# Optimization experiments

Hardware: AMD Instinct MI355X
Metric: run time of the kernel (lower is better)

The kernel has to match this reference:

```python
import jax, jax.numpy as jnp
import numpy as np

N_NODES = 100000
N_EDGES = 1600000
D_FEAT = 128
N_CLASS = 40
K_HOPS = 2  # nlayers


def setup_inputs() -> dict:
    key = jax.random.key(0)
    k1, k2, k3, k4, k5 = jax.random.split(key, 5)
    src = jax.random.randint(k1, (N_EDGES,), 0, N_NODES)
    dst = jax.random.randint(k2, (N_EDGES,), 0, N_NODES)
    features = jax.random.normal(k3, (N_NODES, D_FEAT), dtype=jnp.float32)
    # positive edge weights (EdgeWeightNorm requires nonnegative)
    edge_weight = jax.random.uniform(k4, (N_EDGES,), dtype=jnp.float32, minval=0.1, maxval=1.0)
    W = jax.random.normal(k5, (D_FEAT, N_CLASS), dtype=jnp.float32) / np.float32(np.sqrt(D_FEAT))
    b = jnp.zeros((N_CLASS,), dtype=jnp.float32)
    return {"features": features, "src": src, "dst": dst,
            "edge_weight": edge_weight, "W": W, "b": b}


def reference(features, src, dst, edge_weight, W, b):
    """SGConv (DGL) with edge_weight: EdgeWeightNorm('both') then k SpMM hops, then fc."""
    n = features.shape[0]
    # EdgeWeightNorm('both'): w_ij / sqrt(out_deg_w(src_i) * in_deg_w(dst_j))
    out_deg = jax.ops.segment_sum(edge_weight, src, num_segments=n)  # weighted out-degree
    in_deg = jax.ops.segment_sum(edge_weight, dst, num_segments=n)   # weighted in-degree
    w = edge_weight * jax.lax.rsqrt(out_deg[src]) * jax.lax.rsqrt(in_deg[dst])  # [E]
    h = features
    for _ in range(K_HOPS):
        # message = h[src] * w ; aggregate = scatter-sum over dst
        h = jax.ops.segment_sum(h[src] * w[:, None], dst, num_segments=n)  # [N, D]
    return h @ W + b  # fc projection [N, C]
```

## Files before the change

### kernel.cpp

```cpp
#include <hip/hip_runtime.h>

#define N_NODES 100000
#define N_EDGES 1600000
#define D_FEAT  128
#define N_CLASS 40
#define ELL_CAP 48

#define QS  10239.6875f
#define DQ  9.765923e-5f
#define FSC  2048.0f
#define FINV (1.0f/2048.0f)
#define CNT_SHIFT 20
#define W_MASK ((1u << CNT_SHIFT) - 1u)

#define RSZ 20000
#define NR 5
#define SLICES 32
#define EPS (N_EDGES/SLICES)
#define HB (NR*SLICES)

#define GEMM4_T ((N_NODES/4)*(N_CLASS/4))
#define GEMM4_B ((GEMM4_T + 1023)/1024)

#define NCH 5

__device__ __forceinline__ float bf_lo(unsigned int u) { return __uint_as_float(u << 16); }
__device__ __forceinline__ float bf_hi(unsigned int u) { return __uint_as_float(u & 0xFFFF0000u); }
__device__ __forceinline__ unsigned int bf_pack2(float a, float b) {
    unsigned int ua = __float_as_uint(a), ub = __float_as_uint(b);
    ua = (ua + 0x7FFFu + ((ua >> 16) & 1u)) >> 16;
    ub = (ub + 0x7FFFu + ((ub >> 16) & 1u)) & 0xFFFF0000u;
    return ua | ub;
}

__global__ __launch_bounds__(1024, 8) void mega1_kernel(
    const int* __restrict__ src, const int* __restrict__ dst, const float* __restrict__ ew,
    const float* __restrict__ f, const float* __restrict__ W,
    unsigned int* __restrict__ dhist, unsigned int* __restrict__ shist,
    unsigned int* __restrict__ g0)
{
    __shared__ unsigned int smem[RSZ];
    const int b = blockIdx.x;
    const int tid = threadIdx.x;

    if (b < 2 * HB) {
        const bool isDst = (b < HB);
        const int b2 = isDst ? b : b - HB;
        const int* idxarr = isDst ? dst : src;
        unsigned int* outh = isDst ? dhist : shist;
        int r = b2 / SLICES, s = b2 - r * SLICES;
        int nb = r * RSZ;
        for (int i = tid; i < RSZ; i += 1024) smem[i] = 0u;
        __syncthreads();
        int e0 = s * EPS;
        const int4*   idx4 = (const int4*)(idxarr + e0);
        const float4* ew4  = (const float4*)(ew + e0);
        const unsigned int cbit = isDst ? (1u << CNT_SHIFT) : 0u;
        for (int i = tid; i < EPS / 8; i += 1024) {
            int4   ia = idx4[2 * i],     ib = idx4[2 * i + 1];
            float4 wa = ew4[2 * i],      wb = ew4[2 * i + 1];
            unsigned int r0 = (unsigned int)(ia.x - nb);
            unsigned int r1 = (unsigned int)(ia.y - nb);
            unsigned int r2 = (unsigned int)(ia.z - nb);
            unsigned int r3 = (unsigned int)(ia.w - nb);
            unsigned int r4 = (unsigned int)(ib.x - nb);
            unsigned int r5 = (unsigned int)(ib.y - nb);
            unsigned int r6 = (unsigned int)(ib.z - nb);
            unsigned int r7 = (unsigned int)(ib.w - nb);
            if (r0 < RSZ) atomicAdd(&smem[r0], cbit | (unsigned int)(wa.x * FSC + 0.5f));
            if (r1 < RSZ) atomicAdd(&smem[r1], cbit | (unsigned int)(wa.y * FSC + 0.5f));
            if (r2 < RSZ) atomicAdd(&smem[r2], cbit | (unsigned int)(wa.z * FSC + 0.5f));
            if (r3 < RSZ) atomicAdd(&smem[r3], cbit | (unsigned int)(wa.w * FSC + 0.5f));
            if (r4 < RSZ) atomicAdd(&smem[r4], cbit | (unsigned int)(wb.x * FSC + 0.5f));
            if (r5 < RSZ) atomicAdd(&smem[r5], cbit | (unsigned int)(wb.y * FSC + 0.5f));
            if (r6 < RSZ) atomicAdd(&smem[r6], cbit | (unsigned int)(wb.z * FSC + 0.5f));
            if (r7 < RSZ) atomicAdd(&smem[r7], cbit | (unsigned int)(wb.w * FSC + 0.5f));
        }
        __syncthreads();
        unsigned int* o = outh + (size_t)b2 * RSZ;
        for (int i = tid; i < RSZ; i += 1024) o[i] = smem[i];
    } else {
        float* Ws = (float*)smem;
        for (int i = tid; i < D_FEAT * N_CLASS; i += 1024) Ws[i] = W[i];
        __syncthreads();
        int idx = (b - 2 * HB) * 1024 + tid;
        if (idx >= GEMM4_T) return;
        int n4 = idx / (N_CLASS / 4);
        int c4i = idx - n4 * (N_CLASS / 4);
        int c4 = c4i * 4;
        int n0 = n4 * 4;
        const float* fr0 = f + (size_t)n0 * D_FEAT;
        float4 acc0 = {0.f, 0.f, 0.f, 0.f};
        float4 acc1 = {0.f, 0.f, 0.f, 0.f};
        float4 acc2 = {0.f, 0.f, 0.f, 0.f};
        float4 acc3 = {0.f, 0.f, 0.f, 0.f};
#pragma unroll 1
        for (int kq = 0; kq < D_FEAT; kq += 4) {
            float4 fv0 = *(const float4*)(fr0 + kq);
            float4 fv1 = *(const float4*)(fr0 + D_FEAT + kq);
            float4 fv2 = *(const float4*)(fr0 + 2 * D_FEAT + kq);
            float4 fv3 = *(const float4*)(fr0 + 3 * D_FEAT + kq);
#pragma unroll
            for (int j = 0; j < 4; ++j) {
                float fa = (j == 0) ? fv0.x : (j == 1) ? fv0.y : (j == 2) ? fv0.z : fv0.w;
                float fb = (j == 0) ? fv1.x : (j == 1) ? fv1.y : (j == 2) ? fv1.z : fv1.w;
                float fc = (j == 0) ? fv2.x : (j == 1) ? fv2.y : (j == 2) ? fv2.z : fv2.w;
                float fd = (j == 0) ? fv3.x : (j == 1) ? fv3.y : (j == 2) ? fv3.z : fv3.w;
                const float4 wv = *(const float4*)&Ws[(kq + j) * N_CLASS + c4];
                acc0.x = fmaf(fa, wv.x, acc0.x); acc0.y = fmaf(fa, wv.y, acc0.y);
                acc0.z = fmaf(fa, wv.z, acc0.z); acc0.w = fmaf(fa, wv.w, acc0.w);
                acc1.x = fmaf(fb, wv.x, acc1.x); acc1.y = fmaf(fb, wv.y, acc1.y);
                acc1.z = fmaf(fb, wv.z, acc1.z); acc1.w = fmaf(fb, wv.w, acc1.w);
                acc2.x = fmaf(fc, wv.x, acc2.x); acc2.y = fmaf(fc, wv.y, acc2.y);
                acc2.z = fmaf(fc, wv.z, acc2.z); acc2.w = fmaf(fc, wv.w, acc2.w);
                acc3.x = fmaf(fd, wv.x, acc3.x); acc3.y = fmaf(fd, wv.y, acc3.y);
                acc3.z = fmaf(fd, wv.z, acc3.z); acc3.w = fmaf(fd, wv.w, acc3.w);
            }
        }
        uint2 p0, p1, p2, p3;
        p0.x = bf_pack2(acc0.x, acc0.y); p0.y = bf_pack2(acc0.z, acc0.w);
        p1.x = bf_pack2(acc1.x, acc1.y); p1.y = bf_pack2(acc1.z, acc1.w);
        p2.x = bf_pack2(acc2.x, acc2.y); p2.y = bf_pack2(acc2.z, acc2.w);
        p3.x = bf_pack2(acc3.x, acc3.y); p3.y = bf_pack2(acc3.z, acc3.w);
        *(uint2*)&g0[(size_t)n0 * (N_CLASS / 2) + c4i * 2] = p0;
        *(uint2*)&g0[(size_t)(n0 + 1) * (N_CLASS / 2) + c4i * 2] = p1;
        *(uint2*)&g0[(size_t)(n0 + 2) * (N_CLASS / 2) + c4i * 2] = p2;
        *(uint2*)&g0[(size_t)(n0 + 3) * (N_CLASS / 2) + c4i * 2] = p3;
    }
}

__global__ __launch_bounds__(256) void scan_kernel(
    const unsigned int* __restrict__ dhist, const unsigned int* __restrict__ shist,
    unsigned char* __restrict__ base8, int* __restrict__ cnt,
    float* __restrict__ rs_out, float* __restrict__ rs_in,
    unsigned int* __restrict__ ell)
{
    __shared__ unsigned int owp[256], iwp[256], cntp[256];
    int t = blockIdx.x * 256 + threadIdx.x;
    int n = t >> 2, q = t & 3;
    bool valid = n < N_NODES;
    unsigned int ow = 0, iw = 0, tot = 0;
    unsigned int c0=0,c1=0,c2=0,c3=0,c4=0,c5=0,c6=0,c7=0;
    const unsigned int* dp = nullptr;
    unsigned char* b8 = nullptr;
    if (valid) {
        int r = n / RSZ, off = n - r * RSZ;
        dp = dhist + (size_t)r * SLICES * RSZ + off + (size_t)(q * 8) * RSZ;
        const unsigned int* sp = shist + (size_t)r * SLICES * RSZ + off + (size_t)(q * 8) * RSZ;
        b8 = base8 + (size_t)r * SLICES * RSZ + off + (size_t)(q * 8) * RSZ;
        unsigned int d0 = dp[0],        d1 = dp[(size_t)RSZ],     d2 = dp[(size_t)2*RSZ], d3 = dp[(size_t)3*RSZ];
        unsigned int d4 = dp[(size_t)4*RSZ], d5 = dp[(size_t)5*RSZ], d6 = dp[(size_t)6*RSZ], d7 = dp[(size_t)7*RSZ];
        unsigned int s0 = sp[0],        s1 = sp[(size_t)RSZ],     s2 = sp[(size_t)2*RSZ], s3 = sp[(size_t)3*RSZ];
        unsigned int s4 = sp[(size_t)4*RSZ], s5 = sp[(size_t)5*RSZ], s6 = sp[(size_t)6*RSZ], s7 = sp[(size_t)7*RSZ];
        ow = s0+s1+s2+s3+s4+s5+s6+s7;
        iw = (d0&W_MASK)+(d1&W_MASK)+(d2&W_MASK)+(d3&W_MASK)
           + (d4&W_MASK)+(d5&W_MASK)+(d6&W_MASK)+(d7&W_MASK);
        c0 = d0>>CNT_SHIFT; c1 = d1>>CNT_SHIFT; c2 = d2>>CNT_SHIFT; c3 = d3>>CNT_SHIFT;
        c4 = d4>>CNT_SHIFT; c5 = d5>>CNT_SHIFT; c6 = d6>>CNT_SHIFT; c7 = d7>>CNT_SHIFT;
        tot = c0+c1+c2+c3+c4+c5+c6+c7;
    }
    owp[threadIdx.x] = ow; iwp[threadIdx.x] = iw; cntp[threadIdx.x] = tot;
    __syncthreads();
    if (!valid) return;
    int b0 = threadIdx.x & ~3;
    unsigned int base = 0;
    if (q > 0) base += cntp[b0];
    if (q > 1) base += cntp[b0 + 1];
    if (q > 2) base += cntp[b0 + 2];
    unsigned int p = base;
    b8[0] = (unsigned char)p; p += c0;
    b8[(size_t)RSZ]   = (unsigned char)p; p += c1;
    b8[(size_t)2*RSZ] = (unsigned char)p; p += c2;
    b8[(size_t)3*RSZ] = (unsigned char)p; p += c3;
    b8[(size_t)4*RSZ] = (unsigned char)p; p += c4;
    b8[(size_t)5*RSZ] = (unsigned char)p; p += c5;
    b8[(size_t)6*RSZ] = (unsigned char)p; p += c6;
    b8[(size_t)7*RSZ] = (unsigned char)p;
    if (q == 0) {
        unsigned int owt = owp[b0] + owp[b0+1] + owp[b0+2] + owp[b0+3];
        unsigned int iwt = iwp[b0] + iwp[b0+1] + iwp[b0+2] + iwp[b0+3];
        unsigned int run = cntp[b0] + cntp[b0+1] + cntp[b0+2] + cntp[b0+3];
        rs_out[n] = owt ? rsqrtf((float)owt * FINV) : 0.f;
        rs_in[n]  = iwt ? rsqrtf((float)iwt * FINV) : 0.f;
        cnt[n] = (int)run;
        int k  = min((int)run, ELL_CAP);
        int k8 = min((k + 7) & ~7, ELL_CAP);
        unsigned int* row = ell + (size_t)n * ELL_CAP;
        for (int i = k; i < k8; ++i) row[i] = 0u;
    }
}

__global__ __launch_bounds__(1024) void fill_kernel(
    const int* __restrict__ src, const int* __restrict__ dst, const float* __restrict__ ew,
    const unsigned char* __restrict__ base8, const float* __restrict__ rs_out,
    unsigned int* __restrict__ ell)
{
    __shared__ unsigned int lds[RSZ];
    const int r = blockIdx.x & 7;
    const int s = blockIdx.x >> 3;
    if (r >= NR) return;
    const int tid = threadIdx.x;
    const int b2 = r * SLICES + s;
    int nb = r * RSZ;
    const unsigned int* bp = (const unsigned int*)(base8 + (size_t)b2 * RSZ);
    for (int i = tid; i < RSZ / 4; i += 1024) {
        unsigned int v = bp[i];
        lds[4 * i]     = v & 255u;
        lds[4 * i + 1] = (v >> 8) & 255u;
        lds[4 * i + 2] = (v >> 16) & 255u;
        lds[4 * i + 3] = v >> 24;
    }
    __syncthreads();
    int e0 = s * EPS;
    const int4*   d4 = (const int4*)(dst + e0);
    const int4*   s4 = (const int4*)(src + e0);
    const float4* w4 = (const float4*)(ew + e0);
    for (int i = tid; i < EPS / 8; i += 1024) {
        int4   da = d4[2 * i], db = d4[2 * i + 1];
        int4   sa = s4[2 * i], sb = s4[2 * i + 1];
        float4 wa = w4[2 * i], wb = w4[2 * i + 1];
#pragma unroll
        for (int j = 0; j < 8; ++j) {
            int d, sn; float w;
            switch (j) {
                case 0: d = da.x; sn = sa.x; w = wa.x; break;
                case 1: d = da.y; sn = sa.y; w = wa.y; break;
                case 2: d = da.z; sn = sa.z; w = wa.z; break;
                case 3: d = da.w; sn = sa.w; w = wa.w; break;
                case 4: d = db.x; sn = sb.x; w = wb.x; break;
                case 5: d = db.y; sn = sb.y; w = wb.y; break;
                case 6: d = db.z; sn = sb.z; w = wb.z; break;
                default: d = db.w; sn = sb.w; w = wb.w; break;
            }
            unsigned int rr = (unsigned int)(d - nb);
            if (rr < RSZ) {
                unsigned int slot = atomicAdd(&lds[rr], 1u);
                if (slot < ELL_CAP) {
                    int q = (int)(w * rs_out[sn] * QS + 0.5f);
                    q = q > 32767 ? 32767 : q;
                    ell[(size_t)d * ELL_CAP + slot] = ((unsigned int)sn << 15) | (unsigned int)q;
                }
            }
        }
    }
}

__global__ void hop_kernel(const unsigned int* __restrict__ ell, const int* __restrict__ cnt,
                           const float* __restrict__ rs_in, const unsigned int* __restrict__ gin,
                           void* __restrict__ gout, const float* __restrict__ bias)
{
    int t = blockIdx.x * 256 + threadIdx.x;
    if (t >= N_NODES * NCH) return;
    int n = t / NCH;
    int c8 = t - n * NCH;
    int k = min(cnt[n], ELL_CAP);
    k = (k + 7) & ~7;
    const uint4* row4 = (const uint4*)(ell + (size_t)n * ELL_CAP);
    const uint4* gin4 = (const uint4*)gin;
    float a0 = 0.f, a1 = 0.f, a2 = 0.f, a3 = 0.f, a4 = 0.f, a5 = 0.f, a6 = 0.f, a7 = 0.f;
    for (int i = 0; i < k; i += 8) {
        uint4 v0 = row4[i >> 2];
        uint4 v1 = row4[(i >> 2) + 1];
        unsigned int e0 = v0.x, e1 = v0.y, e2 = v0.z, e3 = v0.w;
        unsigned int e4 = v1.x, e5 = v1.y, e6 = v1.z, e7 = v1.w;
        uint4 g0v = gin4[(size_t)(e0 >> 15) * NCH + c8];
        uint4 g1v = gin4[(size_t)(e1 >> 15) * NCH + c8];
        uint4 g2v = gin4[(size_t)(e2 >> 15) * NCH + c8];
        uint4 g3v = gin4[(size_t)(e3 >> 15) * NCH + c8];
        uint4 g4v = gin4[(size_t)(e4 >> 15) * NCH + c8];
        uint4 g5v = gin4[(size_t)(e5 >> 15) * NCH + c8];
        uint4 g6v = gin4[(size_t)(e6 >> 15) * NCH + c8];
        uint4 g7v = gin4[(size_t)(e7 >> 15) * NCH + c8];
        float w0 = (float)(e0 & 32767u) * DQ;
        float w1 = (float)(e1 & 32767u) * DQ;
        float w2 = (float)(e2 & 32767u) * DQ;
        float w3 = (float)(e3 & 32767u) * DQ;
        float w4 = (float)(e4 & 32767u) * DQ;
        float w5 = (float)(e5 & 32767u) * DQ;
        float w6 = (float)(e6 & 32767u) * DQ;
        float w7 = (float)(e7 & 32767u) * DQ;
        a0 = fmaf(w0, bf_lo(g0v.x), a0); a1 = fmaf(w0, bf_hi(g0v.x), a1);
        a2 = fmaf(w0, bf_lo(g0v.y), a2); a3 = fmaf(w0, bf_hi(g0v.y), a3);
        a4 = fmaf(w0, bf_lo(g0v.z), a4); a5 = fmaf(w0, bf_hi(g0v.z), a5);
        a6 = fmaf(w0, bf_lo(g0v.w), a6); a7 = fmaf(w0, bf_hi(g0v.w), a7);
        a0 = fmaf(w1, bf_lo(g1v.x), a0); a1 = fmaf(w1, bf_hi(g1v.x), a1);
        a2 = fmaf(w1, bf_lo(g1v.y), a2); a3 = fmaf(w1, bf_hi(g1v.y), a3);
        a4 = fmaf(w1, bf_lo(g1v.z), a4); a5 = fmaf(w1, bf_hi(g1v.z), a5);
        a6 = fmaf(w1, bf_lo(g1v.w), a6); a7 = fmaf(w1, bf_hi(g1v.w), a7);
        a0 = fmaf(w2, bf_lo(g2v.x), a0); a1 = fmaf(w2, bf_hi(g2v.x), a1);
        a2 = fmaf(w2, bf_lo(g2v.y), a2); a3 = fmaf(w2, bf_hi(g2v.y), a3);
        a4 = fmaf(w2, bf_lo(g2v.z), a4); a5 = fmaf(w2, bf_hi(g2v.z), a5);
        a6 = fmaf(w2, bf_lo(g2v.w), a6); a7 = fmaf(w2, bf_hi(g2v.w), a7);
        a0 = fmaf(w3, bf_lo(g3v.x), a0); a1 = fmaf(w3, bf_hi(g3v.x), a1);
        a2 = fmaf(w3, bf_lo(g3v.y), a2); a3 = fmaf(w3, bf_hi(g3v.y), a3);
        a4 = fmaf(w3, bf_lo(g3v.z), a4); a5 = fmaf(w3, bf_hi(g3v.z), a5);
        a6 = fmaf(w3, bf_lo(g3v.w), a6); a7 = fmaf(w3, bf_hi(g3v.w), a7);
        a0 = fmaf(w4, bf_lo(g4v.x), a0); a1 = fmaf(w4, bf_hi(g4v.x), a1);
        a2 = fmaf(w4, bf_lo(g4v.y), a2); a3 = fmaf(w4, bf_hi(g4v.y), a3);
        a4 = fmaf(w4, bf_lo(g4v.z), a4); a5 = fmaf(w4, bf_hi(g4v.z), a5);
        a6 = fmaf(w4, bf_lo(g4v.w), a6); a7 = fmaf(w4, bf_hi(g4v.w), a7);
        a0 = fmaf(w5, bf_lo(g5v.x), a0); a1 = fmaf(w5, bf_hi(g5v.x), a1);
        a2 = fmaf(w5, bf_lo(g5v.y), a2); a3 = fmaf(w5, bf_hi(g5v.y), a3);
        a4 = fmaf(w5, bf_lo(g5v.z), a4); a5 = fmaf(w5, bf_hi(g5v.z), a5);
        a6 = fmaf(w5, bf_lo(g5v.w), a6); a7 = fmaf(w5, bf_hi(g5v.w), a7);
        a0 = fmaf(w6, bf_lo(g6v.x), a0); a1 = fmaf(w6, bf_hi(g6v.x), a1);
        a2 = fmaf(w6, bf_lo(g6v.y), a2); a3 = fmaf(w6, bf_hi(g6v.y), a3);
        a4 = fmaf(w6, bf_lo(g6v.z), a4); a5 = fmaf(w6, bf_hi(g6v.z), a5);
        a6 = fmaf(w6, bf_lo(g6v.w), a6); a7 = fmaf(w6, bf_hi(g6v.w), a7);
        a0 = fmaf(w7, bf_lo(g7v.x), a0); a1 = fmaf(w7, bf_hi(g7v.x), a1);
        a2 = fmaf(w7, bf_lo(g7v.y), a2); a3 = fmaf(w7, bf_hi(g7v.y), a3);
        a4 = fmaf(w7, bf_lo(g7v.z), a4); a5 = fmaf(w7, bf_hi(g7v.z), a5);
        a6 = fmaf(w7, bf_lo(g7v.w), a6); a7 = fmaf(w7, bf_hi(g7v.w), a7);
    }
    float sc = rs_in[n];
    a0 *= sc; a1 *= sc; a2 *= sc; a3 *= sc; a4 *= sc; a5 *= sc; a6 *= sc; a7 *= sc;
    if (bias) {
        const float4 b0 = *(const float4*)&bias[c8 * 8];
        const float4 b1 = *(const float4*)&bias[c8 * 8 + 4];
        float4 o0 = {a0 + b0.x, a1 + b0.y, a2 + b0.z, a3 + b0.w};
        float4 o1 = {a4 + b1.x, a5 + b1.y, a6 + b1.z, a7 + b1.w};
        float* op = (float*)gout + (size_t)n * N_CLASS + c8 * 8;
        *(float4*)op = o0;
        *(float4*)(op + 4) = o1;
    } else {
        uint4 p;
        p.x = bf_pack2(a0, a1);
        p.y = bf_pack2(a2, a3);
        p.z = bf_pack2(a4, a5);
        p.w = bf_pack2(a6, a7);
        ((uint4*)gout)[(size_t)n * NCH + c8] = p;
    }
}

extern "C" void kernel_launch(void* const* d_in, const int* in_sizes, int n_in,
                              void* d_out, int out_size, void* d_ws, size_t ws_size,
                              hipStream_t stream) {
    const float* features = (const float*)d_in[0];
    const int*   src      = (const int*)d_in[1];
    const int*   dst      = (const int*)d_in[2];
    const float* ew       = (const float*)d_in[3];
    const float* W        = (const float*)d_in[4];
    const float* b        = (const float*)d_in[5];
    float*       out      = (float*)d_out;

    char* ws = (char*)d_ws;
    unsigned int* dhist = (unsigned int*)ws;  ws += (size_t)HB * RSZ * 4;
    unsigned int* shist = (unsigned int*)ws;  ws += (size_t)HB * RSZ * 4;
    unsigned char* base8 = (unsigned char*)ws; ws += (size_t)HB * RSZ;
    int*   cnt    = (int*)ws;    ws += (size_t)N_NODES * 4;
    float* rs_out = (float*)ws;  ws += (size_t)N_NODES * 4;
    float* rs_in  = (float*)ws;  ws += (size_t)N_NODES * 4;
    unsigned int* ell = (unsigned int*)ws; ws += (size_t)N_NODES * ELL_CAP * 4;
    unsigned int* g0  = (unsigned int*)ws;
    unsigned int* g1  = dhist;

    const int B = 256;

    mega1_kernel<<<2 * HB + GEMM4_B, 1024, 0, stream>>>(
        src, dst, ew, features, W, dhist, shist, g0);
    scan_kernel<<<(N_NODES * 4 + B - 1) / B, B, 0, stream>>>(
        dhist, shist, base8, cnt, rs_out, rs_in, ell);
    fill_kernel<<<8 * SLICES, 1024, 0, stream>>>(src, dst, ew, base8, rs_out, ell);

    const int HOP_BLOCKS = (N_NODES * NCH + B - 1) / B;
    hop_kernel<<<HOP_BLOCKS, B, 0, stream>>>(ell, cnt, rs_in, g0, (void*)g1, nullptr);
    hop_kernel<<<HOP_BLOCKS, B, 0, stream>>>(ell, cnt, rs_in, g1, (void*)out, b);
}
```

Baseline: 271.9 us.

## Move feature GEMM from histogram kernel into ELL fill kernel

The dense features×W projection is moved out of the histogram kernel and co-scheduled with the ELL fill kernel as extra blocks, so its work overlaps the atomic-heavy fill instead of the histogram pass. Each GEMM thread now computes 2 node rows instead of 4, doubling the GEMM block count for more parallelism. The histogram kernel also drops its occupancy hint in launch_bounds. The trade-off is that the fill kernel carries extra LDS and register pressure from the GEMM branch.

```diff
diff --git a/kernel.cpp b/kernel.cpp
--- a/kernel.cpp
+++ b/kernel.cpp
@@ -19,8 +19,10 @@
 #define EPS (N_EDGES/SLICES)
 #define HB (NR*SLICES)
 
-#define GEMM4_T ((N_NODES/4)*(N_CLASS/4))
-#define GEMM4_B ((GEMM4_T + 1023)/1024)
+#define GEMM2_T ((N_NODES/2)*(N_CLASS/4))
+#define GEMM2_B ((GEMM2_T + 1023)/1024)
+
+#define FILLB 256
 
 #define NCH 5
 
@@ -33,100 +35,48 @@
     return ua | ub;
 }
 
-__global__ __launch_bounds__(1024, 8) void mega1_kernel(
+__global__ __launch_bounds__(1024) void mega1_kernel(
     const int* __restrict__ src, const int* __restrict__ dst, const float* __restrict__ ew,
-    const float* __restrict__ f, const float* __restrict__ W,
-    unsigned int* __restrict__ dhist, unsigned int* __restrict__ shist,
-    unsigned int* __restrict__ g0)
+    unsigned int* __restrict__ dhist, unsigned int* __restrict__ shist)
 {
     __shared__ unsigned int smem[RSZ];
     const int b = blockIdx.x;
     const int tid = threadIdx.x;
-
-    if (b < 2 * HB) {
-        const bool isDst = (b < HB);
-        const int b2 = isDst ? b : b - HB;
-        const int* idxarr = isDst ? dst : src;
-        unsigned int* outh = isDst ? dhist : shist;
-        int r = b2 / SLICES, s = b2 - r * SLICES;
-        int nb = r * RSZ;
-        for (int i = tid; i < RSZ; i += 1024) smem[i] = 0u;
-        __syncthreads();
-        int e0 = s * EPS;
-        const int4*   idx4 = (const int4*)(idxarr + e0);
-        const float4* ew4  = (const float4*)(ew + e0);
-        const unsigned int cbit = isDst ? (1u << CNT_SHIFT) : 0u;
-        for (int i = tid; i < EPS / 8; i += 1024) {
-            int4   ia = idx4[2 * i],     ib = idx4[2 * i + 1];
-            float4 wa = ew4[2 * i],      wb = ew4[2 * i + 1];
-            unsigned int r0 = (unsigned int)(ia.x - nb);
-            unsigned int r1 = (unsigned int)(ia.y - nb);
-            unsigned int r2 = (unsigned int)(ia.z - nb);
-            unsigned int r3 = (unsigned int)(ia.w - nb);
-            unsigned int r4 = (unsigned int)(ib.x - nb);
-            unsigned int r5 = (unsigned int)(ib.y - nb);
-            unsigned int r6 = (unsigned int)(ib.z - nb);
-            unsigned int r7 = (unsigned int)(ib.w - nb);
-            if (r0 < RSZ) atomicAdd(&smem[r0], cbit | (unsigned int)(wa.x * FSC + 0.5f));
-            if (r1 < RSZ) atomicAdd(&smem[r1], cbit | (unsigned int)(wa.y * FSC + 0.5f));
-            if (r2 < RSZ) atomicAdd(&smem[r2], cbit | (unsigned int)(wa.z * FSC + 0.5f));
-            if (r3 < RSZ) atomicAdd(&smem[r3], cbit | (unsigned int)(wa.w * FSC + 0.5f));
-            if (r4 < RSZ) atomicAdd(&smem[r4], cbit | (unsigned int)(wb.x * FSC + 0.5f));
-            if (r5 < RSZ) atomicAdd(&smem[r5], cbit | (unsigned int)(wb.y * FSC + 0.5f));
-            if (r6 < RSZ) atomicAdd(&smem[r6], cbit | (unsigned int)(wb.z * FSC + 0.5f));
-            if (r7 < RSZ) atomicAdd(&smem[r7], cbit | (unsigned int)(wb.w * FSC + 0.5f));
-        }
-        __syncthreads();
-        unsigned int* o = outh + (size_t)b2 * RSZ;
-        for (int i = tid; i < RSZ; i += 1024) o[i] = smem[i];
-    } else {
-        float* Ws = (float*)smem;
-        for (int i = tid; i < D_FEAT * N_CLASS; i += 1024) Ws[i] = W[i];
-        __syncthreads();
-        int idx = (b - 2 * HB) * 1024 + tid;
-        if (idx >= GEMM4_T) return;
-        int n4 = idx / (N_CLASS / 4);
-        int c4i = idx - n4 * (N_CLASS / 4);
-        int c4 = c4i * 4;
-        int n0 = n4 * 4;
-        const float* fr0 = f + (size_t)n0 * D_FEAT;
-        float4 acc0 = {0.f, 0.f, 0.f, 0.f};
-        float4 acc1 = {0.f, 0.f, 0.f, 0.f};
-        float4 acc2 = {0.f, 0.f, 0.f, 0.f};
-        float4 acc3 = {0.f, 0.f, 0.f, 0.f};
-#pragma unroll 1
-        for (int kq = 0; kq < D_FEAT; kq += 4) {
-            float4 fv0 = *(const float4*)(fr0 + kq);
-            float4 fv1 = *(const float4*)(fr0 + D_FEAT + kq);
-            float4 fv2 = *(const float4*)(fr0 + 2 * D_FEAT + kq);
-            float4 fv3 = *(const float4*)(fr0 + 3 * D_FEAT + kq);
-#pragma unroll
-            for (int j = 0; j < 4; ++j) {
-                float fa = (j == 0) ? fv0.x : (j == 1) ? fv0.y : (j == 2) ? fv0.z : fv0.w;
-                float fb = (j == 0) ? fv1.x : (j == 1) ? fv1.y : (j == 2) ? fv1.z : fv1.w;
-                float fc = (j == 0) ? fv2.x : (j == 1) ? fv2.y : (j == 2) ? fv2.z : fv2.w;
-                float fd = (j == 0) ? fv3.x : (j == 1) ? fv3.y : (j == 2) ? fv3.z : fv3.w;
-                const float4 wv = *(const float4*)&Ws[(kq + j) * N_CLASS + c4];
-                acc0.x = fmaf(fa, wv.x, acc0.x); acc0.y = fmaf(fa, wv.y, acc0.y);
-                acc0.z = fmaf(fa, wv.z, acc0.z); acc0.w = fmaf(fa, wv.w, acc0.w);
-                acc1.x = fmaf(fb, wv.x, acc1.x); acc1.y = fmaf(fb, wv.y, acc1.y);
-                acc1.z = fmaf(fb, wv.z, acc1.z); acc1.w = fmaf(fb, wv.w, acc1.w);
-                acc2.x = fmaf(fc, wv.x, acc2.x); acc2.y = fmaf(fc, wv.y, acc2.y);
-                acc2.z = fmaf(fc, wv.z, acc2.z); acc2.w = fmaf(fc, wv.w, acc2.w);
-                acc3.x = fmaf(fd, wv.x, acc3.x); acc3.y = fmaf(fd, wv.y, acc3.y);
-                acc3.z = fmaf(fd, wv.z, acc3.z); acc3.w = fmaf(fd, wv.w, acc3.w);
-            }
-        }
-        uint2 p0, p1, p2, p3;
-        p0.x = bf_pack2(acc0.x, acc0.y); p0.y = bf_pack2(acc0.z, acc0.w);
-        p1.x = bf_pack2(acc1.x, acc1.y); p1.y = bf_pack2(acc1.z, acc1.w);
-        p2.x = bf_pack2(acc2.x, acc2.y); p2.y = bf_pack2(acc2.z, acc2.w);
-        p3.x = bf_pack2(acc3.x, acc3.y); p3.y = bf_pack2(acc3.z, acc3.w);
-        *(uint2*)&g0[(size_t)n0 * (N_CLASS / 2) + c4i * 2] = p0;
-        *(uint2*)&g0[(size_t)(n0 + 1) * (N_CLASS / 2) + c4i * 2] = p1;
-        *(uint2*)&g0[(size_t)(n0 + 2) * (N_CLASS / 2) + c4i * 2] = p2;
-        *(uint2*)&g0[(size_t)(n0 + 3) * (N_CLASS / 2) + c4i * 2] = p3;
-    }
+    const bool isDst = (b < HB);
+    const int b2 = isDst ? b : b - HB;
+    const int* idxarr = isDst ? dst : src;
+    unsigned int* outh = isDst ? dhist : shist;
+    int r = b2 / SLICES, s = b2 - r * SLICES;
+    int nb = r * RSZ;
+    for (int i = tid; i < RSZ; i += 1024) smem[i] = 0u;
+    __syncthreads();
+    int e0 = s * EPS;
+    const int4*   idx4 = (const int4*)(idxarr + e0);
+    const float4* ew4  = (const float4*)(ew + e0);
+    const unsigned int cbit = isDst ? (1u << CNT_SHIFT) : 0u;
+    for (int i = tid; i < EPS / 8; i += 1024) {
+        int4   ia = idx4[2 * i],     ib = idx4[2 * i + 1];
+        float4 wa = ew4[2 * i],      wb = ew4[2 * i + 1];
+        unsigned int r0 = (unsigned int)(ia.x - nb);
+        unsigned int r1 = (unsigned int)(ia.y - nb);
+        unsigned int r2 = (unsigned int)(ia.z - nb);
+        unsigned int r3 = (unsigned int)(ia.w - nb);
+        unsigned int r4 = (unsigned int)(ib.x - nb);
+        unsigned int r5 = (unsigned int)(ib.y - nb);
+        unsigned int r6 = (unsigned int)(ib.z - nb);
+        unsigned int r7 = (unsigned int)(ib.w - nb);
+        if (r0 < RSZ) atomicAdd(&smem[r0], cbit | (unsigned int)(wa.x * FSC + 0.5f));
+        if (r1 < RSZ) atomicAdd(&smem[r1], cbit | (unsigned int)(wa.y * FSC + 0.5f));
+        if (r2 < RSZ) atomicAdd(&smem[r2], cbit | (unsigned int)(wa.z * FSC + 0.5f));
+        if (r3 < RSZ) atomicAdd(&smem[r3], cbit | (unsigned int)(wa.w * FSC + 0.5f));
+        if (r4 < RSZ) atomicAdd(&smem[r4], cbit | (unsigned int)(wb.x * FSC + 0.5f));
+        if (r5 < RSZ) atomicAdd(&smem[r5], cbit | (unsigned int)(wb.y * FSC + 0.5f));
+        if (r6 < RSZ) atomicAdd(&smem[r6], cbit | (unsigned int)(wb.z * FSC + 0.5f));
+        if (r7 < RSZ) atomicAdd(&smem[r7], cbit | (unsigned int)(wb.w * FSC + 0.5f));
+    }
+    __syncthreads();
+    unsigned int* o = outh + (size_t)b2 * RSZ;
+    for (int i = tid; i < RSZ; i += 1024) o[i] = smem[i];
 }
 
 __global__ __launch_bounds__(256) void scan_kernel(
@@ -141,11 +91,10 @@
     bool valid = n < N_NODES;
     unsigned int ow = 0, iw = 0, tot = 0;
     unsigned int c0=0,c1=0,c2=0,c3=0,c4=0,c5=0,c6=0,c7=0;
-    const unsigned int* dp = nullptr;
     unsigned char* b8 = nullptr;
     if (valid) {
         int r = n / RSZ, off = n - r * RSZ;
-        dp = dhist + (size_t)r * SLICES * RSZ + off + (size_t)(q * 8) * RSZ;
+        const unsigned int* dp = dhist + (size_t)r * SLICES * RSZ + off + (size_t)(q * 8) * RSZ;
         const unsigned int* sp = shist + (size_t)r * SLICES * RSZ + off + (size_t)(q * 8) * RSZ;
         b8 = base8 + (size_t)r * SLICES * RSZ + off + (size_t)(q * 8) * RSZ;
         unsigned int d0 = dp[0],        d1 = dp[(size_t)RSZ],     d2 = dp[(size_t)2*RSZ], d3 = dp[(size_t)3*RSZ];
@@ -190,58 +139,98 @@
     }
 }
 
-__global__ __launch_bounds__(1024) void fill_kernel(
+__global__ __launch_bounds__(1024) void fill_gemm_kernel(
     const int* __restrict__ src, const int* __restrict__ dst, const float* __restrict__ ew,
     const unsigned char* __restrict__ base8, const float* __restrict__ rs_out,
-    unsigned int* __restrict__ ell)
+    unsigned int* __restrict__ ell,
+    const float* __restrict__ f, const float* __restrict__ W,
+    unsigned int* __restrict__ g0)
 {
     __shared__ unsigned int lds[RSZ];
-    const int r = blockIdx.x & 7;
-    const int s = blockIdx.x >> 3;
-    if (r >= NR) return;
+    const int b = blockIdx.x;
     const int tid = threadIdx.x;
-    const int b2 = r * SLICES + s;
-    int nb = r * RSZ;
-    const unsigned int* bp = (const unsigned int*)(base8 + (size_t)b2 * RSZ);
-    for (int i = tid; i < RSZ / 4; i += 1024) {
-        unsigned int v = bp[i];
-        lds[4 * i]     = v & 255u;
-        lds[4 * i + 1] = (v >> 8) & 255u;
-        lds[4 * i + 2] = (v >> 16) & 255u;
-        lds[4 * i + 3] = v >> 24;
-    }
-    __syncthreads();
-    int e0 = s * EPS;
-    const int4*   d4 = (const int4*)(dst + e0);
-    const int4*   s4 = (const int4*)(src + e0);
-    const float4* w4 = (const float4*)(ew + e0);
-    for (int i = tid; i < EPS / 8; i += 1024) {
-        int4   da = d4[2 * i], db = d4[2 * i + 1];
-        int4   sa = s4[2 * i], sb = s4[2 * i + 1];
-        float4 wa = w4[2 * i], wb = w4[2 * i + 1];
+
+    if (b < FILLB) {
+        const int r = b & 7;
+        const int s = b >> 3;
+        if (r >= NR) return;
+        const int b2 = r * SLICES + s;
+        int nb = r * RSZ;
+        const unsigned int* bp = (const unsigned int*)(base8 + (size_t)b2 * RSZ);
+        for (int i = tid; i < RSZ / 4; i += 1024) {
+            unsigned int v = bp[i];
+            lds[4 * i]     = v & 255u;
+            lds[4 * i + 1] = (v >> 8) & 255u;
+            lds[4 * i + 2] = (v >> 16) & 255u;
+            lds[4 * i + 3] = v >> 24;
+        }
+        __syncthreads();
+        int e0 = s * EPS;
+        const int4*   d4 = (const int4*)(dst + e0);
+        const int4*   s4 = (const int4*)(src + e0);
+        const float4* w4 = (const float4*)(ew + e0);
+        for (int i = tid; i < EPS / 8; i += 1024) {
+            int4   da = d4[2 * i], db = d4[2 * i + 1];
+            int4   sa = s4[2 * i], sb = s4[2 * i + 1];
+            float4 wa = w4[2 * i], wb = w4[2 * i + 1];
 #pragma unroll
-        for (int j = 0; j < 8; ++j) {
-            int d, sn; float w;
-            switch (j) {
-                case 0: d = da.x; sn = sa.x; w = wa.x; break;
-                case 1: d = da.y; sn = sa.y; w = wa.y; break;
-                case 2: d = da.z; sn = sa.z; w = wa.z; break;
-                case 3: d = da.w; sn = sa.w; w = wa.w; break;
-                case 4: d = db.x; sn = sb.x; w = wb.x; break;
-                case 5: d = db.y; sn = sb.y; w = wb.y; break;
-                case 6: d = db.z; sn = sb.z; w = wb.z; break;
-                default: d = db.w; sn = sb.w; w = wb.w; break;
-            }
-            unsigned int rr = (unsigned int)(d - nb);
-            if (rr < RSZ) {
-                unsigned int slot = atomicAdd(&lds[rr], 1u);
-                if (slot < ELL_CAP) {
-                    int q = (int)(w * rs_out[sn] * QS + 0.5f);
-                    q = q > 32767 ? 32767 : q;
-                    ell[(size_t)d * ELL_CAP + slot] = ((unsigned int)sn << 15) | (unsigned int)q;
+            for (int j = 0; j < 8; ++j) {
+                int d, sn; float w;
+                switch (j) {
+                    case 0: d = da.x; sn = sa.x; w = wa.x; break;
+                    case 1: d = da.y; sn = sa.y; w = wa.y; break;
+                    case 2: d = da.z; sn = sa.z; w = wa.z; break;
+                    case 3: d = da.w; sn = sa.w; w = wa.w; break;
+                    case 4: d = db.x; sn = sb.x; w = wb.x; break;
+                    case 5: d = db.y; sn = sb.y; w = wb.y; break;
+                    case 6: d = db.z; sn = sb.z; w = wb.z; break;
+                    default: d = db.w; sn = sb.w; w = wb.w; break;
+                }
+                unsigned int rr = (unsigned int)(d - nb);
+                if (rr < RSZ) {
+                    unsigned int slot = atomicAdd(&lds[rr], 1u);
+                    if (slot < ELL_CAP) {
+                        int q = (int)(w * rs_out[sn] * QS + 0.5f);
+                        q = q > 32767 ? 32767 : q;
+                        ell[(size_t)d * ELL_CAP + slot] = ((unsigned int)sn << 15) | (unsigned int)q;
+                    }
                 }
             }
         }
+    } else {
+        float* Ws = (float*)lds;
+        for (int i = tid; i < D_FEAT * N_CLASS; i += 1024) Ws[i] = W[i];
+        __syncthreads();
+        int idx = (b - FILLB) * 1024 + tid;
+        if (idx >= GEMM2_T) return;
+        int n2 = idx / (N_CLASS / 4);
+        int c4i = idx - n2 * (N_CLASS / 4);
+        int c4 = c4i * 4;
+        int n0 = n2 * 2;
+        const float* fr0 = f + (size_t)n0 * D_FEAT;
+        const float* fr1 = fr0 + D_FEAT;
+        float4 acc0 = {0.f, 0.f, 0.f, 0.f};
+        float4 acc1 = {0.f, 0.f, 0.f, 0.f};
+#pragma unroll 1
+        for (int kq = 0; kq < D_FEAT; kq += 4) {
+            float4 fv0 = *(const float4*)(fr0 + kq);
+            float4 fv1 = *(const float4*)(fr1 + kq);
+#pragma unroll
+            for (int j = 0; j < 4; ++j) {
+                float fa = (j == 0) ? fv0.x : (j == 1) ? fv0.y : (j == 2) ? fv0.z : fv0.w;
+                float fb = (j == 0) ? fv1.x : (j == 1) ? fv1.y : (j == 2) ? fv1.z : fv1.w;
+                const float4 wv = *(const float4*)&Ws[(kq + j) * N_CLASS + c4];
+                acc0.x = fmaf(fa, wv.x, acc0.x); acc0.y = fmaf(fa, wv.y, acc0.y);
+                acc0.z = fmaf(fa, wv.z, acc0.z); acc0.w = fmaf(fa, wv.w, acc0.w);
+                acc1.x = fmaf(fb, wv.x, acc1.x); acc1.y = fmaf(fb, wv.y, acc1.y);
+                acc1.z = fmaf(fb, wv.z, acc1.z); acc1.w = fmaf(fb, wv.w, acc1.w);
+            }
+        }
+        uint2 p0, p1;
+        p0.x = bf_pack2(acc0.x, acc0.y); p0.y = bf_pack2(acc0.z, acc0.w);
+        p1.x = bf_pack2(acc1.x, acc1.y); p1.y = bf_pack2(acc1.z, acc1.w);
+        *(uint2*)&g0[(size_t)n0 * (N_CLASS / 2) + c4i * 2] = p0;
+        *(uint2*)&g0[(size_t)(n0 + 1) * (N_CLASS / 2) + c4i * 2] = p1;
     }
 }
 
@@ -356,11 +345,11 @@
 
     const int B = 256;
 
-    mega1_kernel<<<2 * HB + GEMM4_B, 1024, 0, stream>>>(
-        src, dst, ew, features, W, dhist, shist, g0);
+    mega1_kernel<<<2 * HB, 1024, 0, stream>>>(src, dst, ew, dhist, shist);
     scan_kernel<<<(N_NODES * 4 + B - 1) / B, B, 0, stream>>>(
         dhist, shist, base8, cnt, rs_out, rs_in, ell);
-    fill_kernel<<<8 * SLICES, 1024, 0, stream>>>(src, dst, ew, base8, rs_out, ell);
+    fill_gemm_kernel<<<FILLB + GEMM2_B, 1024, 0, stream>>>(
+        src, dst, ew, base8, rs_out, ell, features, W, g0);
 
     const int HOP_BLOCKS = (N_NODES * NCH + B - 1) / B;
     hop_kernel<<<HOP_BLOCKS, B, 0, stream>>>(ell, cnt, rs_in, g0, (void*)g1, nullptr);
```

New measurement: 275.0 us. About the same (+1.1%).

## Split GEMM out of histogram megakernel and shrink histogram range size

Applied to the files above, without the earlier changes.

Moves the feature-times-W projection out of the fused histogram kernel into its own 256-thread kernel launched after the fill pass. The histogram range size drops from 20000 to 12500 nodes over 8 ranges, so the LDS footprint per block shrinks and the fill kernel's 8-range grid is now fully used. The goal is higher occupancy and lighter LDS pressure for the histogram blocks, at the cost of an extra launch, more histogram blocks that each rescan their edge slice, and the loss of overlap between the GEMM and the histogram work.

```diff
diff --git a/kernel.cpp b/kernel.cpp
--- a/kernel.cpp
+++ b/kernel.cpp
@@ -13,14 +13,14 @@
 #define CNT_SHIFT 20
 #define W_MASK ((1u << CNT_SHIFT) - 1u)
 
-#define RSZ 20000
-#define NR 5
+#define RSZ 12500
+#define NR 8
 #define SLICES 32
 #define EPS (N_EDGES/SLICES)
 #define HB (NR*SLICES)
 
 #define GEMM4_T ((N_NODES/4)*(N_CLASS/4))
-#define GEMM4_B ((GEMM4_T + 1023)/1024)
+#define GEMM4_B ((GEMM4_T + 255)/256)
 
 #define NCH 5
 
@@ -33,100 +33,48 @@
     return ua | ub;
 }
 
-__global__ __launch_bounds__(1024, 8) void mega1_kernel(
+__global__ __launch_bounds__(1024) void mega1_kernel(
     const int* __restrict__ src, const int* __restrict__ dst, const float* __restrict__ ew,
-    const float* __restrict__ f, const float* __restrict__ W,
-    unsigned int* __restrict__ dhist, unsigned int* __restrict__ shist,
-    unsigned int* __restrict__ g0)
+    unsigned int* __restrict__ dhist, unsigned int* __restrict__ shist)
 {
     __shared__ unsigned int smem[RSZ];
     const int b = blockIdx.x;
     const int tid = threadIdx.x;
-
-    if (b < 2 * HB) {
-        const bool isDst = (b < HB);
-        const int b2 = isDst ? b : b - HB;
-        const int* idxarr = isDst ? dst : src;
-        unsigned int* outh = isDst ? dhist : shist;
-        int r = b2 / SLICES, s = b2 - r * SLICES;
-        int nb = r * RSZ;
-        for (int i = tid; i < RSZ; i += 1024) smem[i] = 0u;
-        __syncthreads();
-        int e0 = s * EPS;
-        const int4*   idx4 = (const int4*)(idxarr + e0);
-        const float4* ew4  = (const float4*)(ew + e0);
-        const unsigned int cbit = isDst ? (1u << CNT_SHIFT) : 0u;
-        for (int i = tid; i < EPS / 8; i += 1024) {
-            int4   ia = idx4[2 * i],     ib = idx4[2 * i + 1];
-            float4 wa = ew4[2 * i],      wb = ew4[2 * i + 1];
-            unsigned int r0 = (unsigned int)(ia.x - nb);
-            unsigned int r1 = (unsigned int)(ia.y - nb);
-            unsigned int r2 = (unsigned int)(ia.z - nb);
-            unsigned int r3 = (unsigned int)(ia.w - nb);
-            unsigned int r4 = (unsigned int)(ib.x - nb);
-            unsigned int r5 = (unsigned int)(ib.y - nb);
-            unsigned int r6 = (unsigned int)(ib.z - nb);
-            unsigned int r7 = (unsigned int)(ib.w - nb);
-            if (r0 < RSZ) atomicAdd(&smem[r0], cbit | (unsigned int)(wa.x * FSC + 0.5f));
-            if (r1 < RSZ) atomicAdd(&smem[r1], cbit | (unsigned int)(wa.y * FSC + 0.5f));
-            if (r2 < RSZ) atomicAdd(&smem[r2], cbit | (unsigned int)(wa.z * FSC + 0.5f));
-            if (r3 < RSZ) atomicAdd(&smem[r3], cbit | (unsigned int)(wa.w * FSC + 0.5f));
-            if (r4 < RSZ) atomicAdd(&smem[r4], cbit | (unsigned int)(wb.x * FSC + 0.5f));
-            if (r5 < RSZ) atomicAdd(&smem[r5], cbit | (unsigned int)(wb.y * FSC + 0.5f));
-            if (r6 < RSZ) atomicAdd(&smem[r6], cbit | (unsigned int)(wb.z * FSC + 0.5f));
-            if (r7 < RSZ) atomicAdd(&smem[r7], cbit | (unsigned int)(wb.w * FSC + 0.5f));
-        }
-        __syncthreads();
-        unsigned int* o = outh + (size_t)b2 * RSZ;
-        for (int i = tid; i < RSZ; i += 1024) o[i] = smem[i];
-    } else {
-        float* Ws = (float*)smem;
-        for (int i = tid; i < D_FEAT * N_CLASS; i += 1024) Ws[i] = W[i];
-        __syncthreads();
-        int idx = (b - 2 * HB) * 1024 + tid;
-        if (idx >= GEMM4_T) return;
-        int n4 = idx / (N_CLASS / 4);
-        int c4i = idx - n4 * (N_CLASS / 4);
-        int c4 = c4i * 4;
-        int n0 = n4 * 4;
-        const float* fr0 = f + (size_t)n0 * D_FEAT;
-        float4 acc0 = {0.f, 0.f, 0.f, 0.f};
-        float4 acc1 = {0.f, 0.f, 0.f, 0.f};
-        float4 acc2 = {0.f, 0.f, 0.f, 0.f};
-        float4 acc3 = {0.f, 0.f, 0.f, 0.f};
-#pragma unroll 1
-        for (int kq = 0; kq < D_FEAT; kq += 4) {
-            float4 fv0 = *(const float4*)(fr0 + kq);
-            float4 fv1 = *(const float4*)(fr0 + D_FEAT + kq);
-            float4 fv2 = *(const float4*)(fr0 + 2 * D_FEAT + kq);
-            float4 fv3 = *(const float4*)(fr0 + 3 * D_FEAT + kq);
-#pragma unroll
-            for (int j = 0; j < 4; ++j) {
-                float fa = (j == 0) ? fv0.x : (j == 1) ? fv0.y : (j == 2) ? fv0.z : fv0.w;
-                float fb = (j == 0) ? fv1.x : (j == 1) ? fv1.y : (j == 2) ? fv1.z : fv1.w;
-                float fc = (j == 0) ? fv2.x : (j == 1) ? fv2.y : (j == 2) ? fv2.z : fv2.w;
-                float fd = (j == 0) ? fv3.x : (j == 1) ? fv3.y : (j == 2) ? fv3.z : fv3.w;
-                const float4 wv = *(const float4*)&Ws[(kq + j) * N_CLASS + c4];
-                acc0.x = fmaf(fa, wv.x, acc0.x); acc0.y = fmaf(fa, wv.y, acc0.y);
-                acc0.z = fmaf(fa, wv.z, acc0.z); acc0.w = fmaf(fa, wv.w, acc0.w);
-                acc1.x = fmaf(fb, wv.x, acc1.x); acc1.y = fmaf(fb, wv.y, acc1.y);
-                acc1.z = fmaf(fb, wv.z, acc1.z); acc1.w = fmaf(fb, wv.w, acc1.w);
-                acc2.x = fmaf(fc, wv.x, acc2.x); acc2.y = fmaf(fc, wv.y, acc2.y);
-                acc2.z = fmaf(fc, wv.z, acc2.z); acc2.w = fmaf(fc, wv.w, acc2.w);
-                acc3.x = fmaf(fd, wv.x, acc3.x); acc3.y = fmaf(fd, wv.y, acc3.y);
-                acc3.z = fmaf(fd, wv.z, acc3.z); acc3.w = fmaf(fd, wv.w, acc3.w);
-            }
-        }
-        uint2 p0, p1, p2, p3;
-        p0.x = bf_pack2(acc0.x, acc0.y); p0.y = bf_pack2(acc0.z, acc0.w);
-        p1.x = bf_pack2(acc1.x, acc1.y); p1.y = bf_pack2(acc1.z, acc1.w);
-        p2.x = bf_pack2(acc2.x, acc2.y); p2.y = bf_pack2(acc2.z, acc2.w);
-        p3.x = bf_pack2(acc3.x, acc3.y); p3.y = bf_pack2(acc3.z, acc3.w);
-        *(uint2*)&g0[(size_t)n0 * (N_CLASS / 2) + c4i * 2] = p0;
-        *(uint2*)&g0[(size_t)(n0 + 1) * (N_CLASS / 2) + c4i * 2] = p1;
-        *(uint2*)&g0[(size_t)(n0 + 2) * (N_CLASS / 2) + c4i * 2] = p2;
-        *(uint2*)&g0[(size_t)(n0 + 3) * (N_CLASS / 2) + c4i * 2] = p3;
-    }
+    const bool isDst = (b < HB);
+    const int b2 = isDst ? b : b - HB;
+    const int* idxarr = isDst ? dst : src;
+    unsigned int* outh = isDst ? dhist : shist;
+    int r = b2 / SLICES, s = b2 - r * SLICES;
+    int nb = r * RSZ;
+    for (int i = tid; i < RSZ; i += 1024) smem[i] = 0u;
+    __syncthreads();
+    int e0 = s * EPS;
+    const int4*   idx4 = (const int4*)(idxarr + e0);
+    const float4* ew4  = (const float4*)(ew + e0);
+    const unsigned int cbit = isDst ? (1u << CNT_SHIFT) : 0u;
+    for (int i = tid; i < EPS / 8; i += 1024) {
+        int4   ia = idx4[2 * i],     ib = idx4[2 * i + 1];
+        float4 wa = ew4[2 * i],      wb = ew4[2 * i + 1];
+        unsigned int r0 = (unsigned int)(ia.x - nb);
+        unsigned int r1 = (unsigned int)(ia.y - nb);
+        unsigned int r2 = (unsigned int)(ia.z - nb);
+        unsigned int r3 = (unsigned int)(ia.w - nb);
+        unsigned int r4 = (unsigned int)(ib.x - nb);
+        unsigned int r5 = (unsigned int)(ib.y - nb);
+        unsigned int r6 = (unsigned int)(ib.z - nb);
+        unsigned int r7 = (unsigned int)(ib.w - nb);
+        if (r0 < RSZ) atomicAdd(&smem[r0], cbit | (unsigned int)(wa.x * FSC + 0.5f));
+        if (r1 < RSZ) atomicAdd(&smem[r1], cbit | (unsigned int)(wa.y * FSC + 0.5f));
+        if (r2 < RSZ) atomicAdd(&smem[r2], cbit | (unsigned int)(wa.z * FSC + 0.5f));
+        if (r3 < RSZ) atomicAdd(&smem[r3], cbit | (unsigned int)(wa.w * FSC + 0.5f));
+        if (r4 < RSZ) atomicAdd(&smem[r4], cbit | (unsigned int)(wb.x * FSC + 0.5f));
+        if (r5 < RSZ) atomicAdd(&smem[r5], cbit | (unsigned int)(wb.y * FSC + 0.5f));
+        if (r6 < RSZ) atomicAdd(&smem[r6], cbit | (unsigned int)(wb.z * FSC + 0.5f));
+        if (r7 < RSZ) atomicAdd(&smem[r7], cbit | (unsigned int)(wb.w * FSC + 0.5f));
+    }
+    __syncthreads();
+    unsigned int* o = outh + (size_t)b2 * RSZ;
+    for (int i = tid; i < RSZ; i += 1024) o[i] = smem[i];
 }
 
 __global__ __launch_bounds__(256) void scan_kernel(
@@ -140,24 +88,24 @@
     int n = t >> 2, q = t & 3;
     bool valid = n < N_NODES;
     unsigned int ow = 0, iw = 0, tot = 0;
-    unsigned int c0=0,c1=0,c2=0,c3=0,c4=0,c5=0,c6=0,c7=0;
-    const unsigned int* dp = nullptr;
+    unsigned int dv[8];
     unsigned char* b8 = nullptr;
+#pragma unroll
+    for (int j = 0; j < 8; ++j) dv[j] = 0u;
     if (valid) {
         int r = n / RSZ, off = n - r * RSZ;
-        dp = dhist + (size_t)r * SLICES * RSZ + off + (size_t)(q * 8) * RSZ;
+        const unsigned int* dp = dhist + (size_t)r * SLICES * RSZ + off + (size_t)(q * 8) * RSZ;
         const unsigned int* sp = shist + (size_t)r * SLICES * RSZ + off + (size_t)(q * 8) * RSZ;
         b8 = base8 + (size_t)r * SLICES * RSZ + off + (size_t)(q * 8) * RSZ;
-        unsigned int d0 = dp[0],        d1 = dp[(size_t)RSZ],     d2 = dp[(size_t)2*RSZ], d3 = dp[(size_t)3*RSZ];
-        unsigned int d4 = dp[(size_t)4*RSZ], d5 = dp[(size_t)5*RSZ], d6 = dp[(size_t)6*RSZ], d7 = dp[(size_t)7*RSZ];
-        unsigned int s0 = sp[0],        s1 = sp[(size_t)RSZ],     s2 = sp[(size_t)2*RSZ], s3 = sp[(size_t)3*RSZ];
-        unsigned int s4 = sp[(size_t)4*RSZ], s5 = sp[(size_t)5*RSZ], s6 = sp[(size_t)6*RSZ], s7 = sp[(size_t)7*RSZ];
-        ow = s0+s1+s2+s3+s4+s5+s6+s7;
-        iw = (d0&W_MASK)+(d1&W_MASK)+(d2&W_MASK)+(d3&W_MASK)
-           + (d4&W_MASK)+(d5&W_MASK)+(d6&W_MASK)+(d7&W_MASK);
-        c0 = d0>>CNT_SHIFT; c1 = d1>>CNT_SHIFT; c2 = d2>>CNT_SHIFT; c3 = d3>>CNT_SHIFT;
-        c4 = d4>>CNT_SHIFT; c5 = d5>>CNT_SHIFT; c6 = d6>>CNT_SHIFT; c7 = d7>>CNT_SHIFT;
-        tot = c0+c1+c2+c3+c4+c5+c6+c7;
+        unsigned int sv[8];
+#pragma unroll
+        for (int j = 0; j < 8; ++j) dv[j] = dp[(size_t)j * RSZ];
+#pragma unroll
+        for (int j = 0; j < 8; ++j) sv[j] = sp[(size_t)j * RSZ];
+#pragma unroll
+        for (int j = 0; j < 8; ++j) ow += sv[j];
+#pragma unroll
+        for (int j = 0; j < 8; ++j) { iw += dv[j] & W_MASK; tot += dv[j] >> CNT_SHIFT; }
     }
     owp[threadIdx.x] = ow; iwp[threadIdx.x] = iw; cntp[threadIdx.x] = tot;
     __syncthreads();
@@ -168,14 +116,11 @@
     if (q > 1) base += cntp[b0 + 1];
     if (q > 2) base += cntp[b0 + 2];
     unsigned int p = base;
-    b8[0] = (unsigned char)p; p += c0;
-    b8[(size_t)RSZ]   = (unsigned char)p; p += c1;
-    b8[(size_t)2*RSZ] = (unsigned char)p; p += c2;
-    b8[(size_t)3*RSZ] = (unsigned char)p; p += c3;
-    b8[(size_t)4*RSZ] = (unsigned char)p; p += c4;
-    b8[(size_t)5*RSZ] = (unsigned char)p; p += c5;
-    b8[(size_t)6*RSZ] = (unsigned char)p; p += c6;
-    b8[(size_t)7*RSZ] = (unsigned char)p;
+#pragma unroll
+    for (int j = 0; j < 8; ++j) {
+        b8[(size_t)j * RSZ] = (unsigned char)p;
+        p += dv[j] >> CNT_SHIFT;
+    }
     if (q == 0) {
         unsigned int owt = owp[b0] + owp[b0+1] + owp[b0+2] + owp[b0+3];
         unsigned int iwt = iwp[b0] + iwp[b0+1] + iwp[b0+2] + iwp[b0+3];
@@ -198,7 +143,6 @@
     __shared__ unsigned int lds[RSZ];
     const int r = blockIdx.x & 7;
     const int s = blockIdx.x >> 3;
-    if (r >= NR) return;
     const int tid = threadIdx.x;
     const int b2 = r * SLICES + s;
     int nb = r * RSZ;
@@ -243,6 +187,59 @@
             }
         }
     }
+}
+
+__global__ __launch_bounds__(256) void gemm_kernel(
+    const float* __restrict__ f, const float* __restrict__ W,
+    unsigned int* __restrict__ g0)
+{
+    __shared__ float Ws[D_FEAT * N_CLASS];
+    const int tid = threadIdx.x;
+    for (int i = tid; i < D_FEAT * N_CLASS; i += 256) Ws[i] = W[i];
+    __syncthreads();
+    int idx = blockIdx.x * 256 + tid;
+    if (idx >= GEMM4_T) return;
+    int n4 = idx / (N_CLASS / 4);
+    int c4i = idx - n4 * (N_CLASS / 4);
+    int c4 = c4i * 4;
+    int n0 = n4 * 4;
+    const float* fr0 = f + (size_t)n0 * D_FEAT;
+    float4 acc0 = {0.f, 0.f, 0.f, 0.f};
+    float4 acc1 = {0.f, 0.f, 0.f, 0.f};
+    float4 acc2 = {0.f, 0.f, 0.f, 0.f};
+    float4 acc3 = {0.f, 0.f, 0.f, 0.f};
+#pragma unroll 1
+    for (int kq = 0; kq < D_FEAT; kq += 4) {
+        float4 fv0 = *(const float4*)(fr0 + kq);
+        float4 fv1 = *(const float4*)(fr0 + D_FEAT + kq);
+        float4 fv2 = *(const float4*)(fr0 + 2 * D_FEAT + kq);
+        float4 fv3 = *(const float4*)(fr0 + 3 * D_FEAT + kq);
+#pragma unroll
+        for (int j = 0; j < 4; ++j) {
+            float fa = (j == 0) ? fv0.x : (j == 1) ? fv0.y : (j == 2) ? fv0.z : fv0.w;
+            float fb = (j == 0) ? fv1.x : (j == 1) ? fv1.y : (j == 2) ? fv1.z : fv1.w;
+            float fc = (j == 0) ? fv2.x : (j == 1) ? fv2.y : (j == 2) ? fv2.z : fv2.w;
+            float fd = (j == 0) ? fv3.x : (j == 1) ? fv3.y : (j == 2) ? fv3.z : fv3.w;
+            const float4 wv = *(const float4*)&Ws[(kq + j) * N_CLASS + c4];
+            acc0.x = fmaf(fa, wv.x, acc0.x); acc0.y = fmaf(fa, wv.y, acc0.y);
+            acc0.z = fmaf(fa, wv.z, acc0.z); acc0.w = fmaf(fa, wv.w, acc0.w);
+            acc1.x = fmaf(fb, wv.x, acc1.x); acc1.y = fmaf(fb, wv.y, acc1.y);
+            acc1.z = fmaf(fb, wv.z, acc1.z); acc1.w = fmaf(fb, wv.w, acc1.w);
+            acc2.x = fmaf(fc, wv.x, acc2.x); acc2.y = fmaf(fc, wv.y, acc2.y);
+            acc2.z = fmaf(fc, wv.z, acc2.z); acc2.w = fmaf(fc, wv.w, acc2.w);
+            acc3.x = fmaf(fd, wv.x, acc3.x); acc3.y = fmaf(fd, wv.y, acc3.y);
+            acc3.z = fmaf(fd, wv.z, acc3.z); acc3.w = fmaf(fd, wv.w, acc3.w);
+        }
+    }
+    uint2 p0, p1, p2, p3;
+    p0.x = bf_pack2(acc0.x, acc0.y); p0.y = bf_pack2(acc0.z, acc0.w);
+    p1.x = bf_pack2(acc1.x, acc1.y); p1.y = bf_pack2(acc1.z, acc1.w);
+    p2.x = bf_pack2(acc2.x, acc2.y); p2.y = bf_pack2(acc2.z, acc2.w);
+    p3.x = bf_pack2(acc3.x, acc3.y); p3.y = bf_pack2(acc3.z, acc3.w);
+    *(uint2*)&g0[(size_t)n0 * (N_CLASS / 2) + c4i * 2] = p0;
+    *(uint2*)&g0[(size_t)(n0 + 1) * (N_CLASS / 2) + c4i * 2] = p1;
+    *(uint2*)&g0[(size_t)(n0 + 2) * (N_CLASS / 2) + c4i * 2] = p2;
+    *(uint2*)&g0[(size_t)(n0 + 3) * (N_CLASS / 2) + c4i * 2] = p3;
 }
 
 __global__ void hop_kernel(const unsigned int* __restrict__ ell, const int* __restrict__ cnt,
@@ -356,11 +353,11 @@
 
     const int B = 256;
 
-    mega1_kernel<<<2 * HB + GEMM4_B, 1024, 0, stream>>>(
-        src, dst, ew, features, W, dhist, shist, g0);
+    mega1_kernel<<<2 * HB, 1024, 0, stream>>>(src, dst, ew, dhist, shist);
     scan_kernel<<<(N_NODES * 4 + B - 1) / B, B, 0, stream>>>(
         dhist, shist, base8, cnt, rs_out, rs_in, ell);
     fill_kernel<<<8 * SLICES, 1024, 0, stream>>>(src, dst, ew, base8, rs_out, ell);
+    gemm_kernel<<<GEMM4_B, B, 0, stream>>>(features, W, g0);
 
     const int HOP_BLOCKS = (N_NODES * NCH + B - 1) / B;
     hop_kernel<<<HOP_BLOCKS, B, 0, stream>>>(ell, cnt, rs_in, g0, (void*)g1, nullptr);
```

Result: faster. 254.2 us, median of 2 (-6.5%).
